# Performance work log

Measured on AMD Instinct MI355X. Metric: run time of the kernel, lower is better.

Reference implementation:

```python
import jax, jax.numpy as jnp
import numpy as np
import math

COV_WEIGHT = 1.0
BANDWIDTH_FACTOR = 1.06
SQRT_2PI = math.sqrt(2.0 * math.pi)
EPS_LOG = 1e-8
H_MIN = 1e-4


def setup_inputs() -> dict:
    key = jax.random.key(0)
    activity = jax.random.normal(key, (2048, 64), dtype=jnp.float32)
    return {"activity": activity}


def reference(activity):
    B, R = activity.shape
    # Silverman bandwidth per receptor (torch .std uses ddof=1)
    std = jnp.std(activity, axis=0, ddof=1)                     # (R,)
    h = jnp.maximum(BANDWIDTH_FACTOR * std * (B ** (-0.2)), H_MIN)  # (R,)

    # Pairwise Gaussian KDE: query == samples == activity
    u = (activity[:, None, :] - activity[None, :, :]) / h       # (B_q, B_s, R)
    kernel_values = jnp.exp(-0.5 * u * u) / SQRT_2PI             # (B_q, B_s, R)
    density = kernel_values.sum(axis=1) / (B * h)                # (B_q, R)

    entropies = -jnp.mean(jnp.log(density + EPS_LOG), axis=0)    # (R,)
    loss_entropy = -entropies.mean()

    # Covariance penalty: sum of squared off-diagonals
    centered = activity - activity.mean(axis=0, keepdims=True)
    cov = (centered.T @ centered) / (B - 1)                      # (R, R)
    off = cov - jnp.diag(jnp.diag(cov))
    loss_cov = jnp.sum(off * off)

    total_loss = loss_entropy + COV_WEIGHT * loss_cov
    return total_loss
```

## Files before the change

### kernel.cpp

```cpp
#include <hip/hip_runtime.h>
#include <math.h>

#define B_SZ 2048
#define R_SZ 64
#define QT 8
#define KDE_BLOCKS (B_SZ / QT)

#define B_POW_NEG02 0.217637640824031f
#define SQRT_2PI 2.5066282746310002f
#define LOG2E 1.44269504088896340736f

extern "C" __device__ float __ocml_native_exp2_f32(float);

typedef __attribute__((ext_vector_type(2))) float f32x2;


__global__ __launch_bounds__(1024) void kde_fused_kernel(const float* __restrict__ A,
                                                         float* __restrict__ density,
                                                         float* __restrict__ ent_acc,
                                                         int* __restrict__ done2) {
    int tid = threadIdx.x;
    int r = tid & 63, sg = tid >> 6;

    float s = 0.f, s2 = 0.f;
    {
        const float* Ac = A + sg * (128 * R_SZ) + r;
#pragma unroll 8
        for (int b = 0; b < 128; ++b) {
            float v = Ac[b * R_SZ];
            s += v;
            s2 = fmaf(v, v, s2);
        }
    }
    __shared__ float sred[16][64], s2red[16][64];
    __shared__ float ksh[64];
    sred[sg][r] = s; s2red[sg][r] = s2;
    __syncthreads();
    if (tid < 64) {
        float S = 0.f, S2 = 0.f;
#pragma unroll
        for (int t = 0; t < 16; ++t) { S += sred[t][tid]; S2 += s2red[t][tid]; }
        float m = S * (1.f / (float)B_SZ);
        float var = (S2 - S * m) * (1.f / (float)(B_SZ - 1));
        var = fmaxf(var, 0.f);
        float h = fmaxf(1.06f * sqrtf(var) * B_POW_NEG02, 1e-4f);
        ksh[tid] = sqrtf(0.5f * LOG2E) / h;
    }
    if (blockIdx.x == 0 && tid == 64) { *ent_acc = 0.f; *done2 = 0; }
    __syncthreads();
    float k = ksh[r];

    int q0 = blockIdx.x * QT;
    f32x2 uq01 = { A[(q0 + 0) * R_SZ + r] * k, A[(q0 + 1) * R_SZ + r] * k };
    f32x2 uq23 = { A[(q0 + 2) * R_SZ + r] * k, A[(q0 + 3) * R_SZ + r] * k };
    f32x2 uq45 = { A[(q0 + 4) * R_SZ + r] * k, A[(q0 + 5) * R_SZ + r] * k };
    f32x2 uq67 = { A[(q0 + 6) * R_SZ + r] * k, A[(q0 + 7) * R_SZ + r] * k };
    f32x2 c01 = { 0.f, 0.f }, c23 = { 0.f, 0.f };
    f32x2 c45 = { 0.f, 0.f }, c67 = { 0.f, 0.f };

#define KDE_BODY(usv)                                                          \
    {                                                                          \
        f32x2 uss = { (usv), (usv) };                                          \
        f32x2 d01 = uq01 - uss, d23 = uq23 - uss;                              \
        f32x2 d45 = uq45 - uss, d67 = uq67 - uss;                              \
        f32x2 n01 = -d01 * d01, n23 = -d23 * d23;                              \
        f32x2 n45 = -d45 * d45, n67 = -d67 * d67;                              \
        f32x2 e01 = { __ocml_native_exp2_f32(n01.x), __ocml_native_exp2_f32(n01.y) }; \
        f32x2 e23 = { __ocml_native_exp2_f32(n23.x), __ocml_native_exp2_f32(n23.y) }; \
        f32x2 e45 = { __ocml_native_exp2_f32(n45.x), __ocml_native_exp2_f32(n45.y) }; \
        f32x2 e67 = { __ocml_native_exp2_f32(n67.x), __ocml_native_exp2_f32(n67.y) }; \
        c01 += e01; c23 += e23; c45 += e45; c67 += e67;                        \
    }

    const float* Up = A + sg * R_SZ + r;
    float p[8];
#pragma unroll
    for (int jj = 0; jj < 8; ++jj) p[jj] = Up[jj * 1024];

    int li = 8 * 1024;
#pragma unroll 1
    for (int kk = 0; kk < 15; ++kk) {
#pragma unroll
        for (int jj = 0; jj < 8; ++jj) {
            float us = p[jj] * k;
            p[jj] = Up[li + jj * 1024];
            KDE_BODY(us);
        }
        li += 8 * 1024;
    }
#pragma unroll
    for (int jj = 0; jj < 8; ++jj) {
        float us = p[jj] * k;
        KDE_BODY(us);
    }
#undef KDE_BODY

    __shared__ float red[16][QT][64];
    red[sg][0][r] = c01.x; red[sg][1][r] = c01.y;
    red[sg][2][r] = c23.x; red[sg][3][r] = c23.y;
    red[sg][4][r] = c45.x; red[sg][5][r] = c45.y;
    red[sg][6][r] = c67.x; red[sg][7][r] = c67.y;
    __syncthreads();
    if (sg < QT) {
        float S = 0.f;
#pragma unroll
        for (int t = 0; t < 16; ++t) S += red[t][sg][r];
        density[(q0 + sg) * R_SZ + r] = S;
    }
}

__global__ __launch_bounds__(1024) void epilogue_kernel(const float* __restrict__ A,
                                                        const float* __restrict__ density,
                                                        float* __restrict__ cov_partial,
                                                        float* __restrict__ ent_acc,
                                                        int* __restrict__ done2,
                                                        float* __restrict__ out) {
    int i = blockIdx.x;
    int tid = threadIdx.x;
    int j = tid & 63, bg = tid >> 6;

    float g = 0.f, sj = 0.f, s2j = 0.f;
#pragma unroll 4
    for (int b = bg; b < B_SZ; b += 16) {
        float ai = A[b * R_SZ + i];
        float aj = A[b * R_SZ + j];
        g = fmaf(ai, aj, g);
        sj += aj;
        s2j = fmaf(aj, aj, s2j);
    }

    __shared__ float gred[16][64], sred[16][64], s2red[16][64];
    __shared__ float gfin[64], sfin[64], lsh[64];
    gred[bg][j] = g; sred[bg][j] = sj; s2red[bg][j] = s2j;
    __syncthreads();
    if (tid < 64) {
        float G = 0.f, S = 0.f, S2 = 0.f;
#pragma unroll
        for (int t = 0; t < 16; ++t) { G += gred[t][j]; S += sred[t][j]; S2 += s2red[t][j]; }
        gfin[j] = G;
        sfin[j] = S;
        float m = S * (1.f / (float)B_SZ);
        float var = (S2 - S * m) * (1.f / (float)(B_SZ - 1));
        var = fmaxf(var, 0.f);
        float h = fmaxf(1.06f * sqrtf(var) * B_POW_NEG02, 1e-4f);
        lsh[j] = 1.0f / ((float)B_SZ * h * SQRT_2PI);
    }
    __syncthreads();
    if (tid < 64) {
        float m_j = sfin[j] * (1.f / (float)B_SZ);
        float m_i = sfin[i] * (1.f / (float)B_SZ);
        float cov = (gfin[j] - (float)B_SZ * m_i * m_j) * (1.f / (float)(B_SZ - 1));
        float v = (j == i) ? 0.f : cov * cov;
        for (int off = 32; off > 0; off >>= 1) v += __shfl_down(v, off, 64);
        if (j == 0) cov_partial[i] = v;
    }

    float ls = lsh[j];
    int f = i * 2048 + tid;
    float v = __logf(fmaf(density[f], ls, 1e-8f))
            + __logf(fmaf(density[f + 1024], ls, 1e-8f));
    for (int off = 32; off > 0; off >>= 1) v += __shfl_down(v, off, 64);
    __shared__ float wr[16];
    if (j == 0) wr[bg] = v;
    __syncthreads();
    __shared__ int lastflag;
    if (tid == 0) {
        float sE = 0.f;
#pragma unroll
        for (int w = 0; w < 16; ++w) sE += wr[w];
        atomicAdd(ent_acc, sE);
        __threadfence();
        int prev = atomicAdd(done2, 1);
        lastflag = (prev == 63);
    }
    __syncthreads();
    if (lastflag && tid < 64) {
        __threadfence();
        float v2 = cov_partial[tid];
        for (int off = 32; off > 0; off >>= 1) v2 += __shfl_down(v2, off, 64);
        if (tid == 0) {
            float ent = __hip_atomic_load(ent_acc, __ATOMIC_ACQUIRE,
                                          __HIP_MEMORY_SCOPE_AGENT);
            out[0] = ent * (1.0f / ((float)B_SZ * (float)R_SZ)) + v2;
        }
    }
}

extern "C" void kernel_launch(void* const* d_in, const int* in_sizes, int n_in,
                              void* d_out, int out_size, void* d_ws, size_t ws_size,
                              hipStream_t stream) {
    const float* A = (const float*)d_in[0];
    float* out = (float*)d_out;

    float* wsf = (float*)d_ws;
    float* cov_partial = wsf;
    float* ent_acc     = wsf + 96;
    int*   done2       = (int*)(wsf + 128);
    float* density     = wsf + 256;

    kde_fused_kernel<<<KDE_BLOCKS, 1024, 0, stream>>>(A, density, ent_acc, done2);
    epilogue_kernel<<<R_SZ, 1024, 0, stream>>>(A, density, cov_partial,
                                               ent_acc, done2, out);
}
```

Baseline: 100.2 us.

## Split prescaling into separate kernel with interleaved layout for float4 sample loads

Moves the per-receptor statistics and bandwidth scaling out of the KDE kernel into a prescale kernel. That kernel writes the scaled activations in a layout that interleaves 4 samples per receptor. The KDE kernel then loads float4 groups of pre-scaled samples, with no per-block column statistics pass and no multiply per sample. This removes the redundant 2048x64 statistics reduction done by each of the 256 blocks, and it cuts the load instruction count. In exchange it adds an extra kernel launch and a write and read of a full-size scaled copy.

```diff
diff --git a/kernel.cpp b/kernel.cpp
--- a/kernel.cpp
+++ b/kernel.cpp
@@ -15,10 +15,11 @@
 typedef __attribute__((ext_vector_type(2))) float f32x2;
 
 
-__global__ __launch_bounds__(1024) void kde_fused_kernel(const float* __restrict__ A,
-                                                         float* __restrict__ density,
-                                                         float* __restrict__ ent_acc,
-                                                         int* __restrict__ done2) {
+__global__ __launch_bounds__(1024) void prescale_kernel(const float* __restrict__ A,
+                                                        float* __restrict__ U2,
+                                                        float* __restrict__ ent_acc,
+                                                        int* __restrict__ done2) {
+    int i = blockIdx.x;
     int tid = threadIdx.x;
     int r = tid & 63, sg = tid >> 6;
 
@@ -46,15 +47,30 @@
         float h = fmaxf(1.06f * sqrtf(var) * B_POW_NEG02, 1e-4f);
         ksh[tid] = sqrtf(0.5f * LOG2E) / h;
     }
-    if (blockIdx.x == 0 && tid == 64) { *ent_acc = 0.f; *done2 = 0; }
-    __syncthreads();
-    float k = ksh[r];
-
+    if (i == 0 && tid == 64) { *ent_acc = 0.f; *done2 = 0; }
+    __syncthreads();
+
+#pragma unroll
+    for (int rep = 0; rep < 2; ++rep) {
+        int dglob = i * 2048 + rep * 1024 + tid;
+        int rr = (dglob >> 2) & 63;
+        int ss = ((dglob >> 8) << 2) | (dglob & 3);
+        U2[dglob] = A[ss * R_SZ + rr] * ksh[rr];
+    }
+}
+
+__global__ __launch_bounds__(1024) void kde_kernel(const float* __restrict__ U2,
+                                                   float* __restrict__ density) {
+    int tid = threadIdx.x;
+    int r = tid & 63, sg = tid >> 6;
     int q0 = blockIdx.x * QT;
-    f32x2 uq01 = { A[(q0 + 0) * R_SZ + r] * k, A[(q0 + 1) * R_SZ + r] * k };
-    f32x2 uq23 = { A[(q0 + 2) * R_SZ + r] * k, A[(q0 + 3) * R_SZ + r] * k };
-    f32x2 uq45 = { A[(q0 + 4) * R_SZ + r] * k, A[(q0 + 5) * R_SZ + r] * k };
-    f32x2 uq67 = { A[(q0 + 6) * R_SZ + r] * k, A[(q0 + 7) * R_SZ + r] * k };
+
+#define QLD(j) U2[((q0 + (j)) >> 2) * 256 + r * 4 + ((q0 + (j)) & 3)]
+    f32x2 uq01 = { QLD(0), QLD(1) };
+    f32x2 uq23 = { QLD(2), QLD(3) };
+    f32x2 uq45 = { QLD(4), QLD(5) };
+    f32x2 uq67 = { QLD(6), QLD(7) };
+#undef QLD
     f32x2 c01 = { 0.f, 0.f }, c23 = { 0.f, 0.f };
     f32x2 c45 = { 0.f, 0.f }, c67 = { 0.f, 0.f };
 
@@ -71,28 +87,27 @@
         f32x2 e67 = { __ocml_native_exp2_f32(n67.x), __ocml_native_exp2_f32(n67.y) }; \
         c01 += e01; c23 += e23; c45 += e45; c67 += e67;                        \
     }
-
-    const float* Up = A + sg * R_SZ + r;
-    float p[8];
-#pragma unroll
-    for (int jj = 0; jj < 8; ++jj) p[jj] = Up[jj * 1024];
-
-    int li = 8 * 1024;
+#define GROUP(v) { KDE_BODY((v).x); KDE_BODY((v).y); KDE_BODY((v).z); KDE_BODY((v).w); }
+
+    const float4* F4 = (const float4*)U2;
+    const float4* Up = F4 + sg * 64 + r;
+    float4 p0 = Up[0];
+    float4 p1 = Up[1024];
+    float4 p2 = Up[2048];
+    float4 p3 = Up[3072];
+
+    int li = 4096;
 #pragma unroll 1
-    for (int kk = 0; kk < 15; ++kk) {
-#pragma unroll
-        for (int jj = 0; jj < 8; ++jj) {
-            float us = p[jj] * k;
-            p[jj] = Up[li + jj * 1024];
-            KDE_BODY(us);
-        }
-        li += 8 * 1024;
-    }
-#pragma unroll
-    for (int jj = 0; jj < 8; ++jj) {
-        float us = p[jj] * k;
-        KDE_BODY(us);
-    }
+    for (int m = 0; m < 7; ++m) {
+        float4 u0 = p0; p0 = Up[li];          GROUP(u0);
+        float4 u1 = p1; p1 = Up[li + 1024];   GROUP(u1);
+        float4 u2 = p2; p2 = Up[li + 2048];   GROUP(u2);
+        float4 u3 = p3; p3 = Up[li + 3072];   GROUP(u3);
+        li += 4096;
+    }
+    GROUP(p0); GROUP(p1); GROUP(p2); GROUP(p3);
+
+#undef GROUP
 #undef KDE_BODY
 
     __shared__ float red[16][QT][64];
@@ -196,9 +211,11 @@
     float* cov_partial = wsf;
     float* ent_acc     = wsf + 96;
     int*   done2       = (int*)(wsf + 128);
-    float* density     = wsf + 256;
-
-    kde_fused_kernel<<<KDE_BLOCKS, 1024, 0, stream>>>(A, density, ent_acc, done2);
+    float* U2          = wsf + 256;
+    float* density     = wsf + 256 + B_SZ * R_SZ;
+
+    prescale_kernel<<<R_SZ, 1024, 0, stream>>>(A, U2, ent_acc, done2);
+    kde_kernel<<<KDE_BLOCKS, 1024, 0, stream>>>(U2, density);
     epilogue_kernel<<<R_SZ, 1024, 0, stream>>>(A, density, cov_partial,
                                                ent_acc, done2, out);
 }
```

Result: slower. 102.3 us (+2.1%).
